# Performance work log

Measured on AMD Instinct MI355X. Metric: run time of the kernel, lower is better.

## Reference

```python
import jax, jax.numpy as jnp
from jax import lax
import numpy as np

MAX_HOP = 10
EPS = 1e-5
NEG_SLOPE = 0.01

def setup_inputs() -> dict:
    key = jax.random.key(0)
    ks = jax.random.split(key, 6)
    B, S, D = 32, 4096, 256
    x = jax.random.normal(ks[0], (B, S, D), jnp.float32)
    mask = jax.random.randint(ks[1], (B, S, 1), 0, 2) == 1
    query = jax.random.normal(ks[2], (D,), jnp.float32)
    conv_w = jax.random.normal(ks[3], (D, D, 5), jnp.float32) * (1.0 / np.sqrt(D * 5))
    conv_b = jnp.zeros((D,), jnp.float32)
    bn_gamma = jnp.ones((D,), jnp.float32)
    bn_beta = jnp.zeros((D,), jnp.float32)
    bn_mean = jnp.zeros((D,), jnp.float32)
    bn_var = jnp.ones((D,), jnp.float32)
    halt_w = jax.random.normal(ks[4], (2, D), jnp.float32) * 0.02
    # bias strongly toward class 0 ("continue") so all MAX_HOP hops execute
    halt_b = jnp.array([5.0, -5.0], jnp.float32)
    return {"x": x, "mask": mask, "query": query, "conv_w": conv_w, "conv_b": conv_b,
            "bn_gamma": bn_gamma, "bn_beta": bn_beta, "bn_mean": bn_mean, "bn_var": bn_var,
            "halt_w": halt_w, "halt_b": halt_b}

def _memnet(x, mask, query, conv_w, conv_b, bn_gamma, bn_beta, bn_mean, bn_var, halt_w, halt_b):
    B = x.shape[0]
    mask2d = mask[..., 0]                       # [B,S]
    q0 = jnp.broadcast_to(query[None, :], (B, query.shape[0]))
    halted0 = jnp.zeros((B,), bool)

    def hop(carry, _):
        xc, q, halted = carry
        # while-loop condition: stop if any halted (checked before the step)
        running = jnp.logical_not(jnp.any(halted))
        e = jnp.einsum('bsd,bd->bs', xc, q)
        e = jnp.where(mask2d, -jnp.inf, e)
        probs = jax.nn.softmax(e, axis=-1)      # [B,S]
        # conv1d (k=5, pad=2) + BatchNorm (eval, running stats) + leaky_relu
        xt = jnp.transpose(xc, (0, 2, 1))       # [B,D,S]
        y = lax.conv_general_dilated(xt, conv_w, (1,), [(2, 2)],
                                     dimension_numbers=('NCH', 'OIH', 'NCH'))
        y = y + conv_b[None, :, None]
        y = (y - bn_mean[None, :, None]) * jax.lax.rsqrt(bn_var + EPS)[None, :, None]
        y = y * bn_gamma[None, :, None] + bn_beta[None, :, None]
        xn = jnp.where(jnp.transpose(y, (0, 2, 1)) >= 0,
                       jnp.transpose(y, (0, 2, 1)),
                       NEG_SLOPE * jnp.transpose(y, (0, 2, 1)))
        xn = jnp.where(mask, 0.0, xn)           # [B,S,D]
        o = jnp.einsum('bsd,bs->bd', xn, probs) # [B,D]
        halt_logits = (o + q) @ halt_w.T + halt_b
        q_new = o + q * (1.0 - halted.astype(xc.dtype))[:, None]
        halted_new = halted | (jnp.argmax(halt_logits, axis=-1) == 1)
        xc = jnp.where(running, xn, xc)
        q = jnp.where(running, q_new, q)
        halted = jnp.where(running, halted_new, halted)
        return (xc, q, halted), None

    (_, q_final, _), _ = lax.scan(hop, (x, q0, halted0), None, length=MAX_HOP)
    return q_final

def reference(x, mask, query, conv_w, conv_b, bn_gamma, bn_beta, bn_mean, bn_var, halt_w, halt_b):
    return _memnet(x, mask, query, conv_w, conv_b, bn_gamma, bn_beta, bn_mean, bn_var, halt_w, halt_b)
```

## Files before the change

### kernel.cpp

```cpp
#include <hip/hip_runtime.h>
#include <hip/hip_bf16.h>
#include <math.h>

#define NB 32
#define NS 4096
#define ND 256
#define NHOP 10
#define EPSBN 1e-5f
#define NEG_SLOPE 0.01f

typedef _Float16 half8 __attribute__((ext_vector_type(8)));
typedef float floatx4 __attribute__((ext_vector_type(4)));

static const size_t SZ_PAIR = (size_t)NB*NS*ND*2;
static const size_t OFF_HI0 = 0;
static const size_t OFF_LO0 = OFF_HI0 + SZ_PAIR;
static const size_t OFF_HI1 = OFF_LO0 + SZ_PAIR;
static const size_t OFF_LO1 = OFF_HI1 + SZ_PAIR;
static const size_t OFF_E   = OFF_LO1 + SZ_PAIR;
static const size_t OFF_Q   = OFF_E   + (size_t)NB*NS*4;
static const size_t OFF_OP  = OFF_Q   + (size_t)NB*ND*4;
static const size_t OFF_WPH = OFF_OP  + (size_t)NB*32*ND*4;
static const size_t OFF_WPL = OFF_WPH + (size_t)1280*ND*2;
static const size_t OFF_SC  = OFF_WPL + (size_t)1280*ND*2;
static const size_t OFF_SH  = OFF_SC  + (size_t)ND*4;
static const size_t OFF_RM  = OFF_SH  + (size_t)ND*4;
static const size_t OFF_RI  = OFF_RM  + (size_t)NB*4;
static const size_t OFF_HA  = OFF_RI  + (size_t)NB*4;
static const size_t OFF_RU  = OFF_HA  + (size_t)NB*4;
static const size_t OFF_ZP  = OFF_RU  + 128;

__device__ __forceinline__ float uh2f(ushort u) {
    _Float16 h = __builtin_bit_cast(_Float16, u);
    return (float)h;
}
__device__ __forceinline__ ushort f2uh(float f) {
    _Float16 h = (_Float16)f;
    return __builtin_bit_cast(ushort, h);
}
__device__ __forceinline__ void load_lds16(const void* g, void* l) {
    __builtin_amdgcn_global_load_lds((const __attribute__((address_space(1))) void*)g,
                                     (__attribute__((address_space(3))) void*)l, 16, 0, 0);
}

__global__ void k_split(const float* __restrict__ x, ushort* __restrict__ hi, ushort* __restrict__ lo)
{
    size_t i = ((size_t)blockIdx.x * 256 + threadIdx.x) * 4;
    float4 v = *(const float4*)(x + i);
    ushort4 h, l;
    h.x = f2uh(v.x); l.x = f2uh(v.x - uh2f(h.x));
    h.y = f2uh(v.y); l.y = f2uh(v.y - uh2f(h.y));
    h.z = f2uh(v.z); l.z = f2uh(v.z - uh2f(h.z));
    h.w = f2uh(v.w); l.w = f2uh(v.w - uh2f(h.w));
    *(ushort4*)(hi + i) = h;
    *(ushort4*)(lo + i) = l;
}

__global__ void k_init(const float* __restrict__ conv_w, const float* __restrict__ conv_b,
                       const float* __restrict__ bn_gamma, const float* __restrict__ bn_beta,
                       const float* __restrict__ bn_mean, const float* __restrict__ bn_var,
                       const float* __restrict__ query,
                       ushort* __restrict__ Wph, ushort* __restrict__ Wpl,
                       float* __restrict__ scale, float* __restrict__ shift,
                       float* __restrict__ q, int* __restrict__ halted, int* __restrict__ running,
                       ushort* __restrict__ zpad)
{
    int idx = blockIdx.x * 256 + threadIdx.x;
    if (idx < 1280 * 256) {
        int dj   = idx & 7;
        int kl   = (idx >> 3) & 3;
        int dout = (idx >> 5) & 255;
        int rest = idx >> 13;
        int ds_  = rest & 1;
        int tkc  = rest >> 1;
        int t    = tkc % 5;
        int kc   = tkc / 5;
        int din  = kc * 64 + ds_ * 32 + kl * 8 + dj;
        float w = conv_w[dout * 1280 + din * 5 + t];
        ushort wh = f2uh(w);
        Wph[idx] = wh;
        Wpl[idx] = f2uh(w - uh2f(wh));
    }
    if (idx < NB * ND) q[idx] = query[idx & (ND - 1)];
    if (idx < ND) {
        float a = bn_gamma[idx] * rsqrtf(bn_var[idx] + EPSBN);
        scale[idx] = a;
        shift[idx] = (conv_b[idx] - bn_mean[idx]) * a + bn_beta[idx];
    }
    if (idx < 128) zpad[idx] = 0;
    if (idx < NB) halted[idx] = 0;
    if (idx == 0) running[0] = 1;
}

__global__ void k_attn(const ushort* __restrict__ xhi, const ushort* __restrict__ xlo,
                       const float* __restrict__ q, const int* __restrict__ mask,
                       float* __restrict__ e)
{
    int row  = blockIdx.x * 4 + (threadIdx.x >> 6);
    int lane = threadIdx.x & 63;
    int b    = row >> 12;
    size_t o = (size_t)row * ND + (lane << 2);
    ushort4 hv = *(const ushort4*)(xhi + o);
    ushort4 lv = *(const ushort4*)(xlo + o);
    float4 qv = *(const float4*)(q + b * ND + (lane << 2));
    float v = (uh2f(hv.x) + uh2f(lv.x)) * qv.x
            + (uh2f(hv.y) + uh2f(lv.y)) * qv.y
            + (uh2f(hv.z) + uh2f(lv.z)) * qv.z
            + (uh2f(hv.w) + uh2f(lv.w)) * qv.w;
    #pragma unroll
    for (int off = 32; off; off >>= 1) v += __shfl_xor(v, off, 64);
    if (lane == 0) e[row] = (mask[row] != 0) ? -INFINITY : v;
}

__global__ void k_stats(const float* __restrict__ e, float* __restrict__ rmax,
                        float* __restrict__ rinv, const int* __restrict__ halted,
                        int* __restrict__ running)
{
    __shared__ float sm[256];
    int b = blockIdx.x, tid = threadIdx.x;
    float m = -INFINITY;
    for (int s = tid; s < NS; s += 256) m = fmaxf(m, e[b * NS + s]);
    sm[tid] = m; __syncthreads();
    for (int off = 128; off; off >>= 1) {
        if (tid < off) sm[tid] = fmaxf(sm[tid], sm[tid + off]);
        __syncthreads();
    }
    float bm = sm[0]; __syncthreads();
    float sum = 0.f;
    for (int s = tid; s < NS; s += 256) sum += expf(e[b * NS + s] - bm);
    sm[tid] = sum; __syncthreads();
    for (int off = 128; off; off >>= 1) {
        if (tid < off) sm[tid] += sm[tid + off];
        __syncthreads();
    }
    if (tid == 0) { rmax[b] = bm; rinv[b] = 1.0f / sm[0]; }
    if (b == 0 && tid < 64) {
        unsigned long long any = __ballot(tid < NB && halted[tid] != 0);
        if (tid == 0) running[0] = (any == 0ull) ? 1 : 0;
    }
}

__global__ __launch_bounds__(256, 2) void k_conv(
    const ushort* __restrict__ xhi, const ushort* __restrict__ xlo,
    ushort* __restrict__ ohi, ushort* __restrict__ olo,
    const ushort* __restrict__ Wph, const ushort* __restrict__ Wpl,
    const float* __restrict__ scale, const float* __restrict__ shift,
    const int* __restrict__ maskp, const float* __restrict__ e,
    const float* __restrict__ rmax, const float* __restrict__ rinv,
    float* __restrict__ o_part, const ushort* __restrict__ zpad,
    const int* __restrict__ running)
{
    const int bb  = blockIdx.x >> 5;
    const int s0  = (blockIdx.x & 31) << 7;
    const int tid = threadIdx.x;

    if (running[0] == 0) {
        const size_t base = ((size_t)bb * NS + s0) * ND;
        const uint4* sh_ = (const uint4*)(xhi + base);
        const uint4* sl_ = (const uint4*)(xlo + base);
        uint4* dh = (uint4*)(ohi + base);
        uint4* dl = (uint4*)(olo + base);
        for (int i = tid; i < 4096; i += 256) { dh[i] = sh_[i]; dl[i] = sl_[i]; }
        return;
    }

    __shared__ __align__(16) char ldsA[2 * 34816];
    __shared__ float p_lds[128];

    const int lane  = tid & 63;
    const int wid   = tid >> 6;
    const int mlane = lane & 15;
    const int klane = lane >> 4;
    const int dbase = wid << 6;

    if (tid < 128) {
        float ev = e[bb * NS + s0 + tid];
        p_lds[tid] = expf(ev - rmax[bb]) * rinv[bb];
    }

    floatx4 acc[8][4];
    #pragma unroll
    for (int m = 0; m < 8; ++m)
        #pragma unroll
        for (int n = 0; n < 4; ++n) acc[m][n] = (floatx4){0.f, 0.f, 0.f, 0.f};

    const int laneoff = (dbase + mlane) * 32 + klane * 8;

    auto STAGE = [&](int buf, int kc) {
        char* bh_ = ldsA + (size_t)buf * 34816;
        char* bl_ = bh_ + 17408;
        for (int i0 = tid; i0 < 1088; i0 += 256) {
            int lrow = i0 >> 3;
            int grp  = (i0 & 7) ^ (lrow & 7);
            int srow = s0 - 2 + lrow;
            const ushort* ph;
            const ushort* pl;
            if (srow >= 0 && srow < NS) {
                size_t go = ((size_t)bb * NS + srow) * ND + (kc << 6) + (grp << 3);
                ph = xhi + go; pl = xlo + go;
            } else {
                ph = zpad + (grp << 3); pl = zpad + (grp << 3);
            }
            load_lds16(ph, bh_ + i0 * 16);
            load_lds16(pl, bl_ + i0 * 16);
        }
    };

    STAGE(0, 0);
    half8 bh[4], bl[4], nbh[4], nbl[4];
    {
        const ushort* wb = Wph + laneoff;
        const ushort* wc = Wpl + laneoff;
        #pragma unroll
        for (int n = 0; n < 4; ++n) {
            bh[n] = *(const half8*)(wb + n * 512);
            bl[n] = *(const half8*)(wc + n * 512);
        }
    }
    asm volatile("s_waitcnt vmcnt(0) lgkmcnt(0)" ::: "memory");
    __builtin_amdgcn_s_barrier();
    asm volatile("" ::: "memory");

    for (int kc = 0; kc < 4; ++kc) {
        const int cur = kc & 1;
        if (kc < 3) STAGE(cur ^ 1, kc + 1);

        const char* Ah = ldsA + cur * 34816;
        const char* Al = Ah + 17408;

        #pragma unroll
        for (int td = 0; td < 10; ++td) {
            const int X = kc * 10 + td;
            {
                const int Xn = (X < 39) ? X + 1 : 39;
                const ushort* wb = Wph + (size_t)Xn * 8192 + laneoff;
                const ushort* wc = Wpl + (size_t)Xn * 8192 + laneoff;
                #pragma unroll
                for (int n = 0; n < 4; ++n) {
                    nbh[n] = *(const half8*)(wb + n * 512);
                    nbl[n] = *(const half8*)(wc + n * 512);
                }
            }
            const int t   = td >> 1;
            const int ds_ = td & 1;
            const int gb  = (ds_ << 2) + klane;

            __builtin_amdgcn_s_setprio(1);
            #pragma unroll
            for (int m = 0; m < 8; ++m) {
                int row = (m << 4) + mlane + t;
                int off = (row << 7) + ((gb ^ (row & 7)) << 4);
                half8 ah = *(const half8*)(Ah + off);
                half8 al = *(const half8*)(Al + off);
                #pragma unroll
                for (int n = 0; n < 4; ++n)
                    acc[m][n] = __builtin_amdgcn_mfma_f32_16x16x32_f16(ah, bh[n], acc[m][n], 0, 0, 0);
                #pragma unroll
                for (int n = 0; n < 4; ++n)
                    acc[m][n] = __builtin_amdgcn_mfma_f32_16x16x32_f16(ah, bl[n], acc[m][n], 0, 0, 0);
                #pragma unroll
                for (int n = 0; n < 4; ++n)
                    acc[m][n] = __builtin_amdgcn_mfma_f32_16x16x32_f16(al, bh[n], acc[m][n], 0, 0, 0);
            }
            __builtin_amdgcn_s_setprio(0);

            #pragma unroll
            for (int n = 0; n < 4; ++n) { bh[n] = nbh[n]; bl[n] = nbl[n]; }
        }

        asm volatile("s_waitcnt vmcnt(0) lgkmcnt(0)" ::: "memory");
        __builtin_amdgcn_s_barrier();
        asm volatile("" ::: "memory");
    }

    float sc[4], sh[4];
    #pragma unroll
    for (int n = 0; n < 4; ++n) {
        int d = dbase + (n << 4) + mlane;
        sc[n] = scale[d]; sh[n] = shift[d];
    }
    float osum[4] = {0.f, 0.f, 0.f, 0.f};
    #pragma unroll
    for (int m = 0; m < 8; ++m) {
        #pragma unroll
        for (int r = 0; r < 4; ++r) {
            int prow = (m << 4) + (klane << 2) + r;
            int s = s0 + prow;
            int mk = maskp[bb * NS + s];
            float po = p_lds[prow];
            size_t ob = ((size_t)bb * NS + s) * ND + dbase + mlane;
            #pragma unroll
            for (int n = 0; n < 4; ++n) {
                float v = acc[m][n][r] * sc[n] + sh[n];
                v = (v >= 0.f) ? v : NEG_SLOPE * v;
                v = mk ? 0.f : v;
                ushort hw = f2uh(v);
                ushort lw = f2uh(v - uh2f(hw));
                ohi[ob + (size_t)(n << 4)] = hw;
                olo[ob + (size_t)(n << 4)] = lw;
                osum[n] += po * v;
            }
        }
    }
    #pragma unroll
    for (int n = 0; n < 4; ++n) {
        osum[n] += __shfl_xor(osum[n], 16, 64);
        osum[n] += __shfl_xor(osum[n], 32, 64);
    }
    if (lane < 16) {
        float* op = o_part + ((size_t)bb * 32 + (s0 >> 7)) * ND;
        #pragma unroll
        for (int n = 0; n < 4; ++n)
            op[dbase + (n << 4) + mlane] = osum[n];
    }
}

__global__ void k_update(const float* __restrict__ o_part, float* __restrict__ q,
                         const float* __restrict__ halt_w, const float* __restrict__ halt_b,
                         int* __restrict__ halted, const int* __restrict__ running)
{
    int b = blockIdx.x, d = threadIdx.x;
    __shared__ float sh0[256], sh1[256];
    float o = 0.f;
    #pragma unroll
    for (int ch = 0; ch < 32; ++ch) o += o_part[(b * 32 + ch) * ND + d];
    float qd = q[b * ND + d];
    float s1 = o + qd;
    sh0[d] = s1 * halt_w[d];
    sh1[d] = s1 * halt_w[ND + d];
    __syncthreads();
    for (int off = 128; off; off >>= 1) {
        if (d < off) { sh0[d] += sh0[d + off]; sh1[d] += sh1[d + off]; }
        __syncthreads();
    }
    float l0 = sh0[0] + halt_b[0];
    float l1 = sh1[0] + halt_b[1];
    int hOld = halted[b];
    if (running[0]) {
        q[b * ND + d] = o + qd * (1.f - (float)hOld);
        if (d == 0) halted[b] = hOld | ((l1 > l0) ? 1 : 0);
    }
}

__global__ void k_copyout(const float* __restrict__ q, float* __restrict__ out)
{
    int idx = blockIdx.x * 256 + threadIdx.x;
    if (idx < NB * ND) out[idx] = q[idx];
}

extern "C" void kernel_launch(void* const* d_in, const int* in_sizes, int n_in,
                              void* d_out, int out_size, void* d_ws, size_t ws_size,
                              hipStream_t stream)
{
    const float* x        = (const float*)d_in[0];
    const int*   mask     = (const int*)  d_in[1];
    const float* query    = (const float*)d_in[2];
    const float* conv_w   = (const float*)d_in[3];
    const float* conv_b   = (const float*)d_in[4];
    const float* bn_gamma = (const float*)d_in[5];
    const float* bn_beta  = (const float*)d_in[6];
    const float* bn_mean  = (const float*)d_in[7];
    const float* bn_var   = (const float*)d_in[8];
    const float* halt_w   = (const float*)d_in[9];
    const float* halt_b   = (const float*)d_in[10];

    char* ws = (char*)d_ws;
    ushort* hi0 = (ushort*)(ws + OFF_HI0);
    ushort* lo0 = (ushort*)(ws + OFF_LO0);
    ushort* hi1 = (ushort*)(ws + OFF_HI1);
    ushort* lo1 = (ushort*)(ws + OFF_LO1);
    float* ebuf = (float*)(ws + OFF_E);
    float* qbuf = (float*)(ws + OFF_Q);
    float* opart= (float*)(ws + OFF_OP);
    ushort* Wph = (ushort*)(ws + OFF_WPH);
    ushort* Wpl = (ushort*)(ws + OFF_WPL);
    float* scale= (float*)(ws + OFF_SC);
    float* shift= (float*)(ws + OFF_SH);
    float* rmax = (float*)(ws + OFF_RM);
    float* rinv = (float*)(ws + OFF_RI);
    int* halted = (int*)  (ws + OFF_HA);
    int* runf   = (int*)  (ws + OFF_RU);
    ushort* zpad= (ushort*)(ws + OFF_ZP);

    k_init<<<1280, 256, 0, stream>>>(conv_w, conv_b, bn_gamma, bn_beta, bn_mean, bn_var,
                                     query, Wph, Wpl, scale, shift, qbuf, halted, runf, zpad);
    k_split<<<32768, 256, 0, stream>>>(x, hi0, lo0);

    for (int h = 0; h < NHOP; ++h) {
        const ushort* ih = (h & 1) ? hi1 : hi0;
        const ushort* il = (h & 1) ? lo1 : lo0;
        ushort* oh = (h & 1) ? hi0 : hi1;
        ushort* ol = (h & 1) ? lo0 : lo1;

        k_attn  <<<NB * NS / 4, 256, 0, stream>>>(ih, il, qbuf, mask, ebuf);
        k_stats <<<NB, 256, 0, stream>>>(ebuf, rmax, rinv, halted, runf);
        k_conv  <<<NB * 32, 256, 0, stream>>>(ih, il, oh, ol, Wph, Wpl, scale, shift,
                                              mask, ebuf, rmax, rinv, opart, zpad, runf);
        k_update<<<NB, 256, 0, stream>>>(opart, qbuf, halt_w, halt_b, halted, runf);
    }

    k_copyout<<<NB, 256, 0, stream>>>(qbuf, (float*)d_out);
}
```

Measured before the change: 2.196 ms.

## Fuse attention scores and softmax into conv kernel with split-softmax partials

Removes the separate attention-score and softmax-stats kernels. Attention dot products are now computed inside the conv kernel from the x tiles already staged in LDS. Each block emits a local max and exp-sum, and the update kernel merges them flash-style with rescaling weights. This avoids a full extra read of the hi/lo x buffers and two kernel launches per hop. In exchange it adds per-block reductions and syncs in the conv kernel, and it double-buffers the halted flags to replace the running flag.

```diff
diff --git a/kernel.cpp b/kernel.cpp
--- a/kernel.cpp
+++ b/kernel.cpp
@@ -17,18 +17,17 @@
 static const size_t OFF_LO0 = OFF_HI0 + SZ_PAIR;
 static const size_t OFF_HI1 = OFF_LO0 + SZ_PAIR;
 static const size_t OFF_LO1 = OFF_HI1 + SZ_PAIR;
-static const size_t OFF_E   = OFF_LO1 + SZ_PAIR;
-static const size_t OFF_Q   = OFF_E   + (size_t)NB*NS*4;
+static const size_t OFF_MP  = OFF_LO1 + SZ_PAIR;
+static const size_t OFF_LP  = OFF_MP  + (size_t)NB*32*4;
+static const size_t OFF_Q   = OFF_LP  + (size_t)NB*32*4;
 static const size_t OFF_OP  = OFF_Q   + (size_t)NB*ND*4;
 static const size_t OFF_WPH = OFF_OP  + (size_t)NB*32*ND*4;
 static const size_t OFF_WPL = OFF_WPH + (size_t)1280*ND*2;
 static const size_t OFF_SC  = OFF_WPL + (size_t)1280*ND*2;
 static const size_t OFF_SH  = OFF_SC  + (size_t)ND*4;
-static const size_t OFF_RM  = OFF_SH  + (size_t)ND*4;
-static const size_t OFF_RI  = OFF_RM  + (size_t)NB*4;
-static const size_t OFF_HA  = OFF_RI  + (size_t)NB*4;
-static const size_t OFF_RU  = OFF_HA  + (size_t)NB*4;
-static const size_t OFF_ZP  = OFF_RU  + 128;
+static const size_t OFF_HA  = OFF_SH  + (size_t)ND*4;
+static const size_t OFF_HB  = OFF_HA  + 128;
+static const size_t OFF_ZP  = OFF_HB  + 128;
 
 __device__ __forceinline__ float uh2f(ushort u) {
     _Float16 h = __builtin_bit_cast(_Float16, u);
@@ -62,7 +61,7 @@
                        const float* __restrict__ query,
                        ushort* __restrict__ Wph, ushort* __restrict__ Wpl,
                        float* __restrict__ scale, float* __restrict__ shift,
-                       float* __restrict__ q, int* __restrict__ halted, int* __restrict__ running,
+                       float* __restrict__ q, int* __restrict__ hA, int* __restrict__ hB,
                        ushort* __restrict__ zpad)
 {
     int idx = blockIdx.x * 256 + threadIdx.x;
@@ -88,56 +87,7 @@
         shift[idx] = (conv_b[idx] - bn_mean[idx]) * a + bn_beta[idx];
     }
     if (idx < 128) zpad[idx] = 0;
-    if (idx < NB) halted[idx] = 0;
-    if (idx == 0) running[0] = 1;
-}
-
-__global__ void k_attn(const ushort* __restrict__ xhi, const ushort* __restrict__ xlo,
-                       const float* __restrict__ q, const int* __restrict__ mask,
-                       float* __restrict__ e)
-{
-    int row  = blockIdx.x * 4 + (threadIdx.x >> 6);
-    int lane = threadIdx.x & 63;
-    int b    = row >> 12;
-    size_t o = (size_t)row * ND + (lane << 2);
-    ushort4 hv = *(const ushort4*)(xhi + o);
-    ushort4 lv = *(const ushort4*)(xlo + o);
-    float4 qv = *(const float4*)(q + b * ND + (lane << 2));
-    float v = (uh2f(hv.x) + uh2f(lv.x)) * qv.x
-            + (uh2f(hv.y) + uh2f(lv.y)) * qv.y
-            + (uh2f(hv.z) + uh2f(lv.z)) * qv.z
-            + (uh2f(hv.w) + uh2f(lv.w)) * qv.w;
-    #pragma unroll
-    for (int off = 32; off; off >>= 1) v += __shfl_xor(v, off, 64);
-    if (lane == 0) e[row] = (mask[row] != 0) ? -INFINITY : v;
-}
-
-__global__ void k_stats(const float* __restrict__ e, float* __restrict__ rmax,
-                        float* __restrict__ rinv, const int* __restrict__ halted,
-                        int* __restrict__ running)
-{
-    __shared__ float sm[256];
-    int b = blockIdx.x, tid = threadIdx.x;
-    float m = -INFINITY;
-    for (int s = tid; s < NS; s += 256) m = fmaxf(m, e[b * NS + s]);
-    sm[tid] = m; __syncthreads();
-    for (int off = 128; off; off >>= 1) {
-        if (tid < off) sm[tid] = fmaxf(sm[tid], sm[tid + off]);
-        __syncthreads();
-    }
-    float bm = sm[0]; __syncthreads();
-    float sum = 0.f;
-    for (int s = tid; s < NS; s += 256) sum += expf(e[b * NS + s] - bm);
-    sm[tid] = sum; __syncthreads();
-    for (int off = 128; off; off >>= 1) {
-        if (tid < off) sm[tid] += sm[tid + off];
-        __syncthreads();
-    }
-    if (tid == 0) { rmax[b] = bm; rinv[b] = 1.0f / sm[0]; }
-    if (b == 0 && tid < 64) {
-        unsigned long long any = __ballot(tid < NB && halted[tid] != 0);
-        if (tid == 0) running[0] = (any == 0ull) ? 1 : 0;
-    }
+    if (idx < NB) { hA[idx] = 0; hB[idx] = 0; }
 }
 
 __global__ __launch_bounds__(256, 2) void k_conv(
@@ -145,38 +95,41 @@
     ushort* __restrict__ ohi, ushort* __restrict__ olo,
     const ushort* __restrict__ Wph, const ushort* __restrict__ Wpl,
     const float* __restrict__ scale, const float* __restrict__ shift,
-    const int* __restrict__ maskp, const float* __restrict__ e,
-    const float* __restrict__ rmax, const float* __restrict__ rinv,
-    float* __restrict__ o_part, const ushort* __restrict__ zpad,
-    const int* __restrict__ running)
+    const int* __restrict__ maskp, const float* __restrict__ q,
+    float* __restrict__ o_part, float* __restrict__ m_part, float* __restrict__ l_part,
+    const ushort* __restrict__ zpad, const int* __restrict__ halted)
 {
     const int bb  = blockIdx.x >> 5;
     const int s0  = (blockIdx.x & 31) << 7;
     const int tid = threadIdx.x;
-
-    if (running[0] == 0) {
-        const size_t base = ((size_t)bb * NS + s0) * ND;
-        const uint4* sh_ = (const uint4*)(xhi + base);
-        const uint4* sl_ = (const uint4*)(xlo + base);
-        uint4* dh = (uint4*)(ohi + base);
-        uint4* dl = (uint4*)(olo + base);
-        for (int i = tid; i < 4096; i += 256) { dh[i] = sh_[i]; dl[i] = sl_[i]; }
-        return;
+    const int lane  = tid & 63;
+
+    {
+        int hv = (lane < NB) ? halted[lane] : 0;
+        unsigned long long bl = __ballot(hv != 0);
+        if (bl != 0ull) {
+            const size_t base = ((size_t)bb * NS + s0) * ND;
+            const uint4* sh_ = (const uint4*)(xhi + base);
+            const uint4* sl_ = (const uint4*)(xlo + base);
+            uint4* dh = (uint4*)(ohi + base);
+            uint4* dl = (uint4*)(olo + base);
+            for (int i = tid; i < 4096; i += 256) { dh[i] = sh_[i]; dl[i] = sl_[i]; }
+            return;
+        }
     }
 
     __shared__ __align__(16) char ldsA[2 * 34816];
     __shared__ float p_lds[128];
-
-    const int lane  = tid & 63;
+    __shared__ float red[128];
+    __shared__ float s_mblk, s_lsum;
+
     const int wid   = tid >> 6;
     const int mlane = lane & 15;
     const int klane = lane >> 4;
     const int dbase = wid << 6;
 
-    if (tid < 128) {
-        float ev = e[bb * NS + s0 + tid];
-        p_lds[tid] = expf(ev - rmax[bb]) * rinv[bb];
-    }
+    const int msk_row = (tid < 128) ? maskp[bb * NS + s0 + tid] : 1;
+    float e_acc = 0.f;
 
     floatx4 acc[8][4];
     #pragma unroll
@@ -227,6 +180,30 @@
 
         const char* Ah = ldsA + cur * 34816;
         const char* Al = Ah + 17408;
+
+        if (tid < 128 && !msk_row) {
+            const int lrow = tid + 2;
+            const int rs = lrow & 7;
+            const float* qp = q + bb * ND + (kc << 6);
+            float ea = 0.f;
+            #pragma unroll
+            for (int g = 0; g < 8; ++g) {
+                int off = (lrow << 7) + ((g ^ rs) << 4);
+                half8 hh = *(const half8*)(Ah + off);
+                half8 ll = *(const half8*)(Al + off);
+                float4 q0 = *(const float4*)(qp + g * 8);
+                float4 q1 = *(const float4*)(qp + g * 8 + 4);
+                ea += ((float)hh[0] + (float)ll[0]) * q0.x;
+                ea += ((float)hh[1] + (float)ll[1]) * q0.y;
+                ea += ((float)hh[2] + (float)ll[2]) * q0.z;
+                ea += ((float)hh[3] + (float)ll[3]) * q0.w;
+                ea += ((float)hh[4] + (float)ll[4]) * q1.x;
+                ea += ((float)hh[5] + (float)ll[5]) * q1.y;
+                ea += ((float)hh[6] + (float)ll[6]) * q1.z;
+                ea += ((float)hh[7] + (float)ll[7]) * q1.w;
+            }
+            e_acc += ea;
+        }
 
         #pragma unroll
         for (int td = 0; td < 10; ++td) {
@@ -273,6 +250,34 @@
         asm volatile("" ::: "memory");
     }
 
+    if (tid < 128) red[tid] = msk_row ? -INFINITY : e_acc;
+    __syncthreads();
+    if (tid < 64) {
+        float v = fmaxf(red[tid], red[tid + 64]);
+        #pragma unroll
+        for (int off = 32; off; off >>= 1) v = fmaxf(v, __shfl_xor(v, off, 64));
+        if (tid == 0) s_mblk = v;
+    }
+    __syncthreads();
+    const float mb = s_mblk;
+    if (tid < 128) {
+        float pt = msk_row ? 0.f : expf(e_acc - mb);
+        p_lds[tid] = pt;
+        red[tid] = pt;
+    }
+    __syncthreads();
+    if (tid < 64) {
+        float v = red[tid] + red[tid + 64];
+        #pragma unroll
+        for (int off = 32; off; off >>= 1) v += __shfl_xor(v, off, 64);
+        if (tid == 0) s_lsum = v;
+    }
+    __syncthreads();
+    if (tid == 0) {
+        m_part[bb * 32 + (s0 >> 7)] = mb;
+        l_part[bb * 32 + (s0 >> 7)] = s_lsum;
+    }
+
     float sc[4], sh[4];
     #pragma unroll
     for (int n = 0; n < 4; ++n) {
@@ -315,15 +320,36 @@
     }
 }
 
-__global__ void k_update(const float* __restrict__ o_part, float* __restrict__ q,
+__global__ void k_update(const float* __restrict__ o_part, const float* __restrict__ m_part,
+                         const float* __restrict__ l_part, float* __restrict__ q,
                          const float* __restrict__ halt_w, const float* __restrict__ halt_b,
-                         int* __restrict__ halted, const int* __restrict__ running)
+                         const int* __restrict__ hIn, int* __restrict__ hOut)
 {
     int b = blockIdx.x, d = threadIdx.x;
+    int lane = d & 63;
+    int hv = (lane < NB) ? hIn[lane] : 0;
+    unsigned long long bl = __ballot(hv != 0);
+    int running = (bl == 0ull) ? 1 : 0;
+
+    __shared__ float w[33];
     __shared__ float sh0[256], sh1[256];
+    if (d == 0) {
+        float M = -INFINITY;
+        for (int ch = 0; ch < 32; ++ch) M = fmaxf(M, m_part[b * 32 + ch]);
+        float S = 0.f;
+        for (int ch = 0; ch < 32; ++ch) {
+            float wv = expf(m_part[b * 32 + ch] - M);
+            w[ch] = wv;
+            S += wv * l_part[b * 32 + ch];
+        }
+        w[32] = 1.0f / S;
+    }
+    __syncthreads();
     float o = 0.f;
     #pragma unroll
-    for (int ch = 0; ch < 32; ++ch) o += o_part[(b * 32 + ch) * ND + d];
+    for (int ch = 0; ch < 32; ++ch) o += w[ch] * o_part[(b * 32 + ch) * ND + d];
+    o *= w[32];
+
     float qd = q[b * ND + d];
     float s1 = o + qd;
     sh0[d] = s1 * halt_w[d];
@@ -335,10 +361,12 @@
     }
     float l0 = sh0[0] + halt_b[0];
     float l1 = sh1[0] + halt_b[1];
-    int hOld = halted[b];
-    if (running[0]) {
+    int hOld = hIn[b];
+    if (running) {
         q[b * ND + d] = o + qd * (1.f - (float)hOld);
-        if (d == 0) halted[b] = hOld | ((l1 > l0) ? 1 : 0);
+        if (d == 0) hOut[b] = hOld | ((l1 > l0) ? 1 : 0);
+    } else {
+        if (d == 0) hOut[b] = hOld;
     }
 }
 
@@ -369,21 +397,20 @@
     ushort* lo0 = (ushort*)(ws + OFF_LO0);
     ushort* hi1 = (ushort*)(ws + OFF_HI1);
     ushort* lo1 = (ushort*)(ws + OFF_LO1);
-    float* ebuf = (float*)(ws + OFF_E);
+    float* mpart= (float*)(ws + OFF_MP);
+    float* lpart= (float*)(ws + OFF_LP);
     float* qbuf = (float*)(ws + OFF_Q);
     float* opart= (float*)(ws + OFF_OP);
     ushort* Wph = (ushort*)(ws + OFF_WPH);
     ushort* Wpl = (ushort*)(ws + OFF_WPL);
     float* scale= (float*)(ws + OFF_SC);
     float* shift= (float*)(ws + OFF_SH);
-    float* rmax = (float*)(ws + OFF_RM);
-    float* rinv = (float*)(ws + OFF_RI);
-    int* halted = (int*)  (ws + OFF_HA);
-    int* runf   = (int*)  (ws + OFF_RU);
+    int* hA     = (int*)  (ws + OFF_HA);
+    int* hB     = (int*)  (ws + OFF_HB);
     ushort* zpad= (ushort*)(ws + OFF_ZP);
 
     k_init<<<1280, 256, 0, stream>>>(conv_w, conv_b, bn_gamma, bn_beta, bn_mean, bn_var,
-                                     query, Wph, Wpl, scale, shift, qbuf, halted, runf, zpad);
+                                     query, Wph, Wpl, scale, shift, qbuf, hA, hB, zpad);
     k_split<<<32768, 256, 0, stream>>>(x, hi0, lo0);
 
     for (int h = 0; h < NHOP; ++h) {
@@ -391,12 +418,12 @@
         const ushort* il = (h & 1) ? lo1 : lo0;
         ushort* oh = (h & 1) ? hi0 : hi1;
         ushort* ol = (h & 1) ? lo0 : lo1;
-
-        k_attn  <<<NB * NS / 4, 256, 0, stream>>>(ih, il, qbuf, mask, ebuf);
-        k_stats <<<NB, 256, 0, stream>>>(ebuf, rmax, rinv, halted, runf);
+        const int* hIn = (h & 1) ? hB : hA;
+        int*       hOut= (h & 1) ? hA : hB;
+
         k_conv  <<<NB * 32, 256, 0, stream>>>(ih, il, oh, ol, Wph, Wpl, scale, shift,
-                                              mask, ebuf, rmax, rinv, opart, zpad, runf);
-        k_update<<<NB, 256, 0, stream>>>(opart, qbuf, halt_w, halt_b, halted, runf);
+                                              mask, qbuf, opart, mpart, lpart, zpad, hIn);
+        k_update<<<NB, 256, 0, stream>>>(opart, mpart, lpart, qbuf, halt_w, halt_b, hIn, hOut);
     }
 
     k_copyout<<<NB, 256, 0, stream>>>(qbuf, (float*)d_out);
```

New measurement: 2.040 ms. 7.1% less time.
